# Kernel optimization log

Hardware: AMD Instinct MI355X
Metric: run time of the kernel (lower is better)

## Reference

```python
import math
import jax, jax.numpy as jnp
import numpy as np

B, S, E, H = 4, 2048, 2048, 16
D = E // H
EPSILON, DELTA, MAX_GRAD_NORM = 1.0, 1e-05, 1.0
# Gaussian mechanism calibration: sigma = C * sqrt(2 ln(1.25/delta)) / epsilon
NOISE_SCALE = MAX_GRAD_NORM * math.sqrt(2.0 * math.log(1.25 / DELTA)) / EPSILON


def _xavier(key, fan_in, fan_out):
    lim = math.sqrt(6.0 / (fan_in + fan_out))
    return jax.random.uniform(key, (fan_out, fan_in), jnp.float32, -lim, lim)


def setup_inputs() -> dict:
    key = jax.random.key(0)
    ks = jax.random.split(key, 8)
    return {
        'query': jax.random.normal(ks[0], (B, S, E), jnp.float32),
        'key_t': jax.random.normal(ks[1], (B, S, E), jnp.float32),
        'value': jax.random.normal(ks[2], (B, S, E), jnp.float32),
        'Wq': _xavier(ks[3], E, E), 'bq': jnp.zeros((E,), jnp.float32),
        'Wk': _xavier(ks[4], E, E), 'bk': jnp.zeros((E,), jnp.float32),
        'Wv': _xavier(ks[5], E, E), 'bv': jnp.zeros((E,), jnp.float32),
        'Wo': _xavier(ks[6], E, E), 'bo': jnp.zeros((E,), jnp.float32),
        'noise': jax.random.normal(ks[7], (B, S, E), jnp.float32),
    }


def reference(query, key_t, value, Wq, bq, Wk, bk, Wv, bv, Wo, bo, noise):
    b, s, e = query.shape
    scale = 1.0 / math.sqrt(D)
    # QKV projections (torch Linear: x @ W.T + b) -> [b, s, H, D]
    q = (query @ Wq.T + bq).reshape(b, s, H, D)
    k = (key_t @ Wk.T + bk).reshape(b, s, H, D)
    v = (value @ Wv.T + bv).reshape(b, s, H, D)
    # attention scores [b, H, s, s]
    scores = jnp.einsum('bqhd,bkhd->bhqk', q, k) * scale
    attn = jax.nn.softmax(scores, axis=-1)
    ctx = jnp.einsum('bhqk,bkhd->bqhd', attn, v).reshape(b, s, e)
    # DP noise injected inside the kernel on the attention output
    ctx = ctx + noise * NOISE_SCALE
    # output projection
    return ctx @ Wo.T + bo
```

## Files before the change

kernel.cpp:

```cpp
#include <hip/hip_runtime.h>
#include <cmath>

#define BATCH 4
#define SEQ   2048
#define EMB   2048
#define NH    16
#define HD    128
#define MDIM  (BATCH*SEQ)
#define KDIM  EMB
#define NDIM  EMB

typedef __bf16 bf16x8 __attribute__((ext_vector_type(8)));
typedef float  f32x4  __attribute__((ext_vector_type(4)));

__device__ __forceinline__ ushort bf16rne(float f) {
  unsigned u = __builtin_bit_cast(unsigned, f);
  u += 0x7fffu + ((u >> 16) & 1u);
  return (ushort)(u >> 16);
}

__global__ __launch_bounds__(256) void cvt_bf16(const float* __restrict__ in,
                                                ushort* __restrict__ out) {
  int i = (blockIdx.x * 256 + threadIdx.x) * 4;
  float4 v = *(const float4*)(in + i);
  ushort4 o;
  o.x = bf16rne(v.x); o.y = bf16rne(v.y); o.z = bf16rne(v.z); o.w = bf16rne(v.w);
  *(ushort4*)(out + i) = o;
}

template<int MODE>
__global__ __launch_bounds__(256, 2)
void gemm_nt(const ushort* __restrict__ A, const ushort* __restrict__ Bm,
             const float* __restrict__ bias, void* __restrict__ out) {
  __shared__ ushort As[128][72];
  __shared__ ushort Bs[128][72];

  const int tid  = threadIdx.x;
  const int wave = tid >> 6, lane = tid & 63;
  const int l15  = lane & 15, quad = lane >> 4;
  const int m0 = blockIdx.x * 128, n0 = blockIdx.y * 128;
  const int wr = (wave >> 1) * 64, wc = (wave & 1) * 64;

  const f32x4 zero4 = {0.f, 0.f, 0.f, 0.f};
  f32x4 acc[4][4];
#pragma unroll
  for (int i = 0; i < 4; ++i)
#pragma unroll
    for (int j = 0; j < 4; ++j) acc[i][j] = zero4;

  for (int kk = 0; kk < KDIM; kk += 64) {
#pragma unroll
    for (int it = 0; it < 4; ++it) {
      int L = it * 256 + tid;
      int row = L >> 3, c8 = (L & 7) * 8;
      int4 va = *(const int4*)(A  + (size_t)(m0 + row) * KDIM + kk + c8);
      int4 vb = *(const int4*)(Bm + (size_t)(n0 + row) * KDIM + kk + c8);
      *(int4*)(&As[row][c8]) = va;
      *(int4*)(&Bs[row][c8]) = vb;
    }
    __syncthreads();
#pragma unroll
    for (int ks = 0; ks < 2; ++ks) {
      bf16x8 af[4], bfr[4];
#pragma unroll
      for (int i = 0; i < 4; ++i)
        af[i] = __builtin_bit_cast(bf16x8, *(const int4*)(&As[wr + i*16 + l15][ks*32 + quad*8]));
#pragma unroll
      for (int j = 0; j < 4; ++j)
        bfr[j] = __builtin_bit_cast(bf16x8, *(const int4*)(&Bs[wc + j*16 + l15][ks*32 + quad*8]));
#pragma unroll
      for (int i = 0; i < 4; ++i)
#pragma unroll
        for (int j = 0; j < 4; ++j)
          acc[i][j] = __builtin_amdgcn_mfma_f32_16x16x32_bf16(af[i], bfr[j], acc[i][j], 0, 0, 0);
    }
    __syncthreads();
  }

  if constexpr (MODE == 0) {
    float* O = (float*)out;
#pragma unroll
    for (int i = 0; i < 4; ++i)
#pragma unroll
      for (int j = 0; j < 4; ++j) {
        int n = n0 + wc + j*16 + l15;
        float bb = bias[n];
#pragma unroll
        for (int r = 0; r < 4; ++r) {
          int m = m0 + wr + i*16 + quad*4 + r;
          O[(size_t)m * NDIM + n] = acc[i][j][r] + bb;
        }
      }
  } else if constexpr (MODE == 1) {
    ushort* O = (ushort*)out;
#pragma unroll
    for (int i = 0; i < 4; ++i)
#pragma unroll
      for (int j = 0; j < 4; ++j) {
        int n = n0 + wc + j*16 + l15;
        float bb = bias[n];
        int h = n >> 7, d = n & 127;
#pragma unroll
        for (int r = 0; r < 4; ++r) {
          int m = m0 + wr + i*16 + quad*4 + r;
          int b = m >> 11, srow = m & 2047;
          O[(((size_t)(b*NH + h) * SEQ + srow) << 7) + d] = bf16rne(acc[i][j][r] + bb);
        }
      }
  } else {
    __shared__ float Tt[4][16][17];
    ushort* O = (ushort*)out;
    const int h = n0 >> 7;
#pragma unroll
    for (int i = 0; i < 4; ++i)
#pragma unroll
      for (int j = 0; j < 4; ++j) {
        int n = n0 + wc + j*16 + l15;
        float bb = bias[n];
#pragma unroll
        for (int r = 0; r < 4; ++r)
          Tt[wave][l15][quad*4 + r] = acc[i][j][r] + bb;
#pragma unroll
        for (int r = 0; r < 4; ++r) {
          int dl = quad*4 + r, sl = l15;
          float v = Tt[wave][dl][sl];
          int m = m0 + wr + i*16 + sl;
          int b = m >> 11, srow = m & 2047;
          int d = wc + j*16 + dl;
          O[((size_t)(b*NH + h) * HD + d) * SEQ + srow] = bf16rne(v);
        }
      }
  }
}

__global__ __launch_bounds__(512, 2)
void attn_kernel(const ushort* __restrict__ Qh, const ushort* __restrict__ Kh,
                 const ushort* __restrict__ Vt, const float* __restrict__ noise,
                 ushort* __restrict__ ctxn, float scale, float ns) {
  __shared__ ushort Ks[64 * 128];
  __shared__ ushort Vs[128 * 64];
  __shared__ ushort Ps[128 * 64];

  const int tid  = threadIdx.x;
  const int wave = tid >> 6, lane = tid & 63;
  const int l15  = lane & 15, quad = lane >> 4;
  const int q0 = blockIdx.x * 128;
  const int bh = blockIdx.y;
  const int b  = bh >> 4, h = bh & 15;

  bf16x8 qf[4];
  {
    const int qrow = q0 + wave*16 + l15;
    const ushort* qp = Qh + ((size_t)bh * SEQ + qrow) * HD;
#pragma unroll
    for (int ks = 0; ks < 4; ++ks)
      qf[ks] = __builtin_bit_cast(bf16x8, *(const int4*)(qp + ks*32 + quad*8));
  }

  const f32x4 zero4 = {0.f, 0.f, 0.f, 0.f};
  f32x4 o[8];
#pragma unroll
  for (int nb = 0; nb < 8; ++nb) o[nb] = zero4;
  float rs[4] = {0.f, 0.f, 0.f, 0.f};

  for (int k0 = 0; k0 < SEQ; k0 += 64) {
#pragma unroll
    for (int it = 0; it < 2; ++it) {
      int L = it * 512 + tid;
      int r = L >> 4, c8 = (L & 15) * 8;
      int4 v = *(const int4*)(Kh + ((size_t)bh * SEQ + k0 + r) * HD + c8);
      *(int4*)(&Ks[r * 128 + (c8 ^ ((r & 7) << 3))]) = v;
    }
#pragma unroll
    for (int it = 0; it < 2; ++it) {
      int L = it * 512 + tid;
      int r = L >> 3, c8 = (L & 7) * 8;
      int4 v = *(const int4*)(Vt + ((size_t)bh * HD + r) * SEQ + k0 + c8);
      *(int4*)(&Vs[r * 64 + (c8 ^ ((r & 7) << 3))]) = v;
    }
    __syncthreads();

#pragma unroll
    for (int ct = 0; ct < 4; ++ct) {
      f32x4 s = zero4;
      const int kr = ct*16 + l15;
      __builtin_amdgcn_s_setprio(1);
#pragma unroll
      for (int ks = 0; ks < 4; ++ks) {
        bf16x8 kf = __builtin_bit_cast(bf16x8,
            *(const int4*)(&Ks[kr * 128 + ((ks*32 + quad*8) ^ ((kr & 7) << 3))]));
        s = __builtin_amdgcn_mfma_f32_16x16x32_bf16(qf[ks], kf, s, 0, 0, 0);
      }
      __builtin_amdgcn_s_setprio(0);
#pragma unroll
      for (int r = 0; r < 4; ++r) {
        float p = __expf(s[r] * scale);
        rs[r] += p;
        int pr = wave*16 + quad*4 + r;
        int pc = ct*16 + l15;
        Ps[pr * 64 + (pc ^ ((pr & 7) << 3))] = bf16rne(p);
      }
    }

    __builtin_amdgcn_s_setprio(1);
#pragma unroll
    for (int ks2 = 0; ks2 < 2; ++ks2) {
      const int par = wave*16 + l15;
      bf16x8 pa = __builtin_bit_cast(bf16x8,
          *(const int4*)(&Ps[par * 64 + ((ks2*32 + quad*8) ^ ((par & 7) << 3))]));
#pragma unroll
      for (int nb = 0; nb < 8; ++nb) {
        const int vr = nb*16 + l15;
        bf16x8 vb = __builtin_bit_cast(bf16x8,
            *(const int4*)(&Vs[vr * 64 + ((ks2*32 + quad*8) ^ ((vr & 7) << 3))]));
        o[nb] = __builtin_amdgcn_mfma_f32_16x16x32_bf16(pa, vb, o[nb], 0, 0, 0);
      }
    }
    __builtin_amdgcn_s_setprio(0);
    __syncthreads();
  }

#pragma unroll
  for (int r = 0; r < 4; ++r) {
    float v = rs[r];
    v += __shfl_xor(v, 1);
    v += __shfl_xor(v, 2);
    v += __shfl_xor(v, 4);
    v += __shfl_xor(v, 8);
    rs[r] = v;
  }

#pragma unroll
  for (int r = 0; r < 4; ++r) {
    float inv = 1.0f / rs[r];
    int sg = q0 + wave*16 + quad*4 + r;
    size_t rowbase = ((size_t)(b * SEQ + sg)) * EMB + h * HD;
#pragma unroll
    for (int nb = 0; nb < 8; ++nb) {
      int e = nb*16 + l15;
      float val = o[nb][r] * inv + noise[rowbase + e] * ns;
      ctxn[rowbase + e] = bf16rne(val);
    }
  }
}

extern "C" void kernel_launch(void* const* d_in, const int* in_sizes, int n_in,
                              void* d_out, int out_size, void* d_ws, size_t ws_size,
                              hipStream_t stream) {
  const float* query = (const float*)d_in[0];
  const float* key_t = (const float*)d_in[1];
  const float* value = (const float*)d_in[2];
  const float* Wq = (const float*)d_in[3];
  const float* bq = (const float*)d_in[4];
  const float* Wk = (const float*)d_in[5];
  const float* bk = (const float*)d_in[6];
  const float* Wv = (const float*)d_in[7];
  const float* bv = (const float*)d_in[8];
  const float* Wo = (const float*)d_in[9];
  const float* bo = (const float*)d_in[10];
  const float* noise = (const float*)d_in[11];

  const size_t SZ_ACT = (size_t)MDIM * KDIM * 2;
  const size_t SZ_W   = (size_t)NDIM * KDIM * 2;
  const size_t need_full = 7 * SZ_ACT + 4 * SZ_W;

  char* p = (char*)d_ws;
  ushort *qb, *kb;
  if (ws_size >= need_full) {
    qb = (ushort*)p; p += SZ_ACT;
    kb = (ushort*)p; p += SZ_ACT;
  } else {
    qb = (ushort*)d_out;
    kb = (ushort*)((char*)d_out + SZ_ACT);
  }
  ushort* vb   = (ushort*)p; p += SZ_ACT;
  ushort* wqb  = (ushort*)p; p += SZ_W;
  ushort* wkb  = (ushort*)p; p += SZ_W;
  ushort* wvb  = (ushort*)p; p += SZ_W;
  ushort* wob  = (ushort*)p; p += SZ_W;
  ushort* Qh   = (ushort*)p; p += SZ_ACT;
  ushort* Kh   = (ushort*)p; p += SZ_ACT;
  ushort* Vt   = (ushort*)p; p += SZ_ACT;
  ushort* ctxn = (ushort*)p; p += SZ_ACT;

  const int nAct = MDIM * KDIM;
  const int nW   = NDIM * KDIM;
  const float NS = (float)sqrt(2.0 * log(1.25 / 1e-5));
  const float SCALE = (float)(1.0 / sqrt((double)HD));

  cvt_bf16<<<dim3(nAct / 1024), dim3(256), 0, stream>>>(query, qb);
  cvt_bf16<<<dim3(nAct / 1024), dim3(256), 0, stream>>>(key_t, kb);
  cvt_bf16<<<dim3(nAct / 1024), dim3(256), 0, stream>>>(value, vb);
  cvt_bf16<<<dim3(nW / 1024),   dim3(256), 0, stream>>>(Wq, wqb);
  cvt_bf16<<<dim3(nW / 1024),   dim3(256), 0, stream>>>(Wk, wkb);
  cvt_bf16<<<dim3(nW / 1024),   dim3(256), 0, stream>>>(Wv, wvb);
  cvt_bf16<<<dim3(nW / 1024),   dim3(256), 0, stream>>>(Wo, wob);

  dim3 ggrid(MDIM / 128, NDIM / 128);
  gemm_nt<1><<<ggrid, dim3(256), 0, stream>>>(qb, wqb, bq, (void*)Qh);
  gemm_nt<1><<<ggrid, dim3(256), 0, stream>>>(kb, wkb, bk, (void*)Kh);
  gemm_nt<2><<<ggrid, dim3(256), 0, stream>>>(vb, wvb, bv, (void*)Vt);

  attn_kernel<<<dim3(SEQ / 128, BATCH * NH), dim3(512), 0, stream>>>(
      Qh, Kh, Vt, noise, ctxn, SCALE, NS);

  gemm_nt<0><<<ggrid, dim3(256), 0, stream>>>(ctxn, wob, bo, d_out);
}
```

Measured before the change: 840.7 us.

## Pipeline GEMM with async global-to-LDS loads, 4-stage buffer, 256x256 tiles

```diff
diff --git a/kernel.cpp b/kernel.cpp
--- a/kernel.cpp
+++ b/kernel.cpp
@@ -19,6 +19,12 @@
   return (ushort)(u >> 16);
 }
 
+__device__ __forceinline__ void gld_lds16(const ushort* g, ushort* l) {
+  __builtin_amdgcn_global_load_lds(
+      (const __attribute__((address_space(1))) unsigned int*)g,
+      (__attribute__((address_space(3))) unsigned int*)l, 16, 0, 0);
+}
+
 __global__ __launch_bounds__(256) void cvt_bf16(const float* __restrict__ in,
                                                 ushort* __restrict__ out) {
   int i = (blockIdx.x * 256 + threadIdx.x) * 4;
@@ -29,105 +35,122 @@
 }
 
 template<int MODE>
-__global__ __launch_bounds__(256, 2)
+__global__ __launch_bounds__(512, 2)
 void gemm_nt(const ushort* __restrict__ A, const ushort* __restrict__ Bm,
              const float* __restrict__ bias, void* __restrict__ out) {
-  __shared__ ushort As[128][72];
-  __shared__ ushort Bs[128][72];
+  __shared__ ushort As[4 * 256 * 32];
+  __shared__ ushort Bs[4 * 256 * 32];
 
   const int tid  = threadIdx.x;
   const int wave = tid >> 6, lane = tid & 63;
   const int l15  = lane & 15, quad = lane >> 4;
-  const int m0 = blockIdx.x * 128, n0 = blockIdx.y * 128;
-  const int wr = (wave >> 1) * 64, wc = (wave & 1) * 64;
+  const int m0 = blockIdx.x * 256, n0 = blockIdx.y * 256;
+  const int wr2 = (wave >> 2) * 128;
+  const int wc2 = (wave & 3) * 64;
 
   const f32x4 zero4 = {0.f, 0.f, 0.f, 0.f};
-  f32x4 acc[4][4];
-#pragma unroll
-  for (int i = 0; i < 4; ++i)
+  f32x4 acc[8][4];
+#pragma unroll
+  for (int i = 0; i < 8; ++i)
 #pragma unroll
     for (int j = 0; j < 4; ++j) acc[i][j] = zero4;
 
-  for (int kk = 0; kk < KDIM; kk += 64) {
-#pragma unroll
-    for (int it = 0; it < 4; ++it) {
-      int L = it * 256 + tid;
-      int row = L >> 3, c8 = (L & 7) * 8;
-      int4 va = *(const int4*)(A  + (size_t)(m0 + row) * KDIM + kk + c8);
-      int4 vb = *(const int4*)(Bm + (size_t)(n0 + row) * KDIM + kk + c8);
-      *(int4*)(&As[row][c8]) = va;
-      *(int4*)(&Bs[row][c8]) = vb;
-    }
-    __syncthreads();
-#pragma unroll
-    for (int ks = 0; ks < 2; ++ks) {
-      bf16x8 af[4], bfr[4];
-#pragma unroll
-      for (int i = 0; i < 4; ++i)
-        af[i] = __builtin_bit_cast(bf16x8, *(const int4*)(&As[wr + i*16 + l15][ks*32 + quad*8]));
+  const int srow = tid >> 2, sc8 = (tid & 3) * 8;
+  const int Lw   = tid & ~63;
+
+  auto STAGE = [&](int c, int t) {
+    const int kk = t * 32;
+#pragma unroll
+    for (int p = 0; p < 2; ++p) {
+      gld_lds16(A  + (size_t)(m0 + p*128 + srow) * KDIM + kk + sc8,
+                As + c*8192 + (p*512 + Lw) * 8);
+      gld_lds16(Bm + (size_t)(n0 + p*128 + srow) * KDIM + kk + sc8,
+                Bs + c*8192 + (p*512 + Lw) * 8);
+    }
+  };
+
+  const int NT = KDIM / 32;
+  STAGE(0, 0); STAGE(1, 1); STAGE(2, 2);
+
+  for (int t = 0; t < NT; ++t) {
+    if (t + 2 < NT)      asm volatile("s_waitcnt vmcnt(8)" ::: "memory");
+    else if (t + 1 < NT) asm volatile("s_waitcnt vmcnt(4)" ::: "memory");
+    else                 asm volatile("s_waitcnt vmcnt(0)" ::: "memory");
+    asm volatile("s_barrier" ::: "memory");
+
+    if (t + 3 < NT) STAGE((t + 3) & 3, t + 3);
+
+    const ushort* Ab = As + (t & 3) * 8192;
+    const ushort* Bb = Bs + (t & 3) * 8192;
+    bf16x8 af[8], bf[4];
+#pragma unroll
+    for (int i = 0; i < 8; ++i)
+      af[i] = __builtin_bit_cast(bf16x8,
+                *(const int4*)(Ab + (wr2 + i*16 + l15) * 32 + quad*8));
+#pragma unroll
+    for (int j = 0; j < 4; ++j)
+      bf[j] = __builtin_bit_cast(bf16x8,
+                *(const int4*)(Bb + (wc2 + j*16 + l15) * 32 + quad*8));
+    __builtin_amdgcn_s_setprio(1);
+#pragma unroll
+    for (int i = 0; i < 8; ++i)
 #pragma unroll
       for (int j = 0; j < 4; ++j)
-        bfr[j] = __builtin_bit_cast(bf16x8, *(const int4*)(&Bs[wc + j*16 + l15][ks*32 + quad*8]));
-#pragma unroll
-      for (int i = 0; i < 4; ++i)
-#pragma unroll
-        for (int j = 0; j < 4; ++j)
-          acc[i][j] = __builtin_amdgcn_mfma_f32_16x16x32_bf16(af[i], bfr[j], acc[i][j], 0, 0, 0);
-    }
-    __syncthreads();
+        acc[i][j] = __builtin_amdgcn_mfma_f32_16x16x32_bf16(af[i], bf[j], acc[i][j], 0, 0, 0);
+    __builtin_amdgcn_s_setprio(0);
   }
 
   if constexpr (MODE == 0) {
     float* O = (float*)out;
 #pragma unroll
-    for (int i = 0; i < 4; ++i)
+    for (int i = 0; i < 8; ++i)
 #pragma unroll
       for (int j = 0; j < 4; ++j) {
-        int n = n0 + wc + j*16 + l15;
+        int n = n0 + wc2 + j*16 + l15;
         float bb = bias[n];
 #pragma unroll
         for (int r = 0; r < 4; ++r) {
-          int m = m0 + wr + i*16 + quad*4 + r;
+          int m = m0 + wr2 + i*16 + quad*4 + r;
           O[(size_t)m * NDIM + n] = acc[i][j][r] + bb;
         }
       }
   } else if constexpr (MODE == 1) {
     ushort* O = (ushort*)out;
 #pragma unroll
-    for (int i = 0; i < 4; ++i)
+    for (int i = 0; i < 8; ++i)
 #pragma unroll
       for (int j = 0; j < 4; ++j) {
-        int n = n0 + wc + j*16 + l15;
+        int n = n0 + wc2 + j*16 + l15;
         float bb = bias[n];
         int h = n >> 7, d = n & 127;
 #pragma unroll
         for (int r = 0; r < 4; ++r) {
-          int m = m0 + wr + i*16 + quad*4 + r;
-          int b = m >> 11, srow = m & 2047;
-          O[(((size_t)(b*NH + h) * SEQ + srow) << 7) + d] = bf16rne(acc[i][j][r] + bb);
+          int m = m0 + wr2 + i*16 + quad*4 + r;
+          int b = m >> 11, sr = m & 2047;
+          O[(((size_t)(b*NH + h) * SEQ + sr) << 7) + d] = bf16rne(acc[i][j][r] + bb);
         }
       }
   } else {
-    __shared__ float Tt[4][16][17];
+    float* TtF = (float*)As;
     ushort* O = (ushort*)out;
-    const int h = n0 >> 7;
-#pragma unroll
-    for (int i = 0; i < 4; ++i)
+#pragma unroll
+    for (int i = 0; i < 8; ++i)
 #pragma unroll
       for (int j = 0; j < 4; ++j) {
-        int n = n0 + wc + j*16 + l15;
+        int n = n0 + wc2 + j*16 + l15;
         float bb = bias[n];
 #pragma unroll
         for (int r = 0; r < 4; ++r)
-          Tt[wave][l15][quad*4 + r] = acc[i][j][r] + bb;
+          TtF[(wave*16 + l15)*17 + quad*4 + r] = acc[i][j][r] + bb;
 #pragma unroll
         for (int r = 0; r < 4; ++r) {
           int dl = quad*4 + r, sl = l15;
-          float v = Tt[wave][dl][sl];
-          int m = m0 + wr + i*16 + sl;
-          int b = m >> 11, srow = m & 2047;
-          int d = wc + j*16 + dl;
-          O[((size_t)(b*NH + h) * HD + d) * SEQ + srow] = bf16rne(v);
+          float v = TtF[(wave*16 + dl)*17 + sl];
+          int m = m0 + wr2 + i*16 + sl;
+          int b = m >> 11, sr = m & 2047;
+          int n2 = n0 + wc2 + j*16 + dl;
+          int h = n2 >> 7, d = n2 & 127;
+          O[((size_t)(b*NH + h) * HD + d) * SEQ + sr] = bf16rne(v);
         }
       }
   }
@@ -296,13 +319,13 @@
   cvt_bf16<<<dim3(nW / 1024),   dim3(256), 0, stream>>>(Wv, wvb);
   cvt_bf16<<<dim3(nW / 1024),   dim3(256), 0, stream>>>(Wo, wob);
 
-  dim3 ggrid(MDIM / 128, NDIM / 128);
-  gemm_nt<1><<<ggrid, dim3(256), 0, stream>>>(qb, wqb, bq, (void*)Qh);
-  gemm_nt<1><<<ggrid, dim3(256), 0, stream>>>(kb, wkb, bk, (void*)Kh);
-  gemm_nt<2><<<ggrid, dim3(256), 0, stream>>>(vb, wvb, bv, (void*)Vt);
+  dim3 ggrid(MDIM / 256, NDIM / 256);
+  gemm_nt<1><<<ggrid, dim3(512), 0, stream>>>(qb, wqb, bq, (void*)Qh);
+  gemm_nt<1><<<ggrid, dim3(512), 0, stream>>>(kb, wkb, bk, (void*)Kh);
+  gemm_nt<2><<<ggrid, dim3(512), 0, stream>>>(vb, wvb, bv, (void*)Vt);
 
   attn_kernel<<<dim3(SEQ / 128, BATCH * NH), dim3(512), 0, stream>>>(
       Qh, Kh, Vt, noise, ctxn, SCALE, NS);
 
-  gemm_nt<0><<<ggrid, dim3(256), 0, stream>>>(ctxn, wob, bo, d_out);
-}
+  gemm_nt<0><<<ggrid, dim3(512), 0, stream>>>(ctxn, wob, bo, d_out);
+}
```

After: 883.7 us. +5.1%, slower.
